# Kernel optimization log

Hardware: AMD Instinct MI355X
Metric: run time of the kernel (lower is better)

## Reference

```python
import jax, jax.numpy as jnp
import numpy as np

D = 1024
H = 16
F = 4096
EPS = 1e-6


def _layernorm(x, alpha, bias):
    # Faithful to torch: unbiased std (ddof=1), divide by (std + eps)
    mean = jnp.mean(x, axis=-1, keepdims=True)
    std = jnp.std(x, axis=-1, keepdims=True, ddof=1)
    return alpha * (x - mean) / (std + EPS) + bias


def setup_inputs() -> dict:
    key = jax.random.key(0)
    ks = jax.random.split(key, 12)
    B, S = 2, 2048
    s = 1.0 / np.sqrt(D)
    inp = {
        "x": jax.random.normal(ks[0], (B, S, D), jnp.float32),
        "mask": jnp.ones((B, 1, 1, S), jnp.int32),
        "wq": jax.random.normal(ks[1], (D, D), jnp.float32) * s,
        "bq": jnp.zeros((D,), jnp.float32),
        "wk": jax.random.normal(ks[2], (D, D), jnp.float32) * s,
        "bk": jnp.zeros((D,), jnp.float32),
        "wv": jax.random.normal(ks[3], (D, D), jnp.float32) * s,
        "bv": jnp.zeros((D,), jnp.float32),
        "wo": jax.random.normal(ks[4], (D, D), jnp.float32) * s,
        "bo": jnp.zeros((D,), jnp.float32),
        "ln1_a": jnp.ones((D,), jnp.float32),
        "ln1_b": jnp.zeros((D,), jnp.float32),
        "ln2_a": jnp.ones((D,), jnp.float32),
        "ln2_b": jnp.zeros((D,), jnp.float32),
        "w1": jax.random.normal(ks[5], (D, F), jnp.float32) * s,
        "b1": jnp.zeros((F,), jnp.float32),
        "w2": jax.random.normal(ks[6], (F, D), jnp.float32) * (1.0 / np.sqrt(F)),
        "b2": jnp.zeros((D,), jnp.float32),
    }
    return inp


def reference(x, mask, wq, bq, wk, bk, wv, bv, wo, bo,
              ln1_a, ln1_b, ln2_a, ln2_b, w1, b1, w2, b2):
    B, S, _ = x.shape
    dk = D // H
    # --- residual 1: pre-LN self-attention ---
    h = _layernorm(x, ln1_a, ln1_b)
    q = (h @ wq + bq).reshape(B, S, H, dk).transpose(0, 2, 1, 3)
    k = (h @ wk + bk).reshape(B, S, H, dk).transpose(0, 2, 1, 3)
    v = (h @ wv + bv).reshape(B, S, H, dk).transpose(0, 2, 1, 3)
    scores = jnp.einsum('bhqd,bhkd->bhqk', q, k) / jnp.sqrt(jnp.float32(dk))
    scores = jnp.where(mask == 0, jnp.float32(-1e9), scores)
    attn = jax.nn.softmax(scores, axis=-1)
    ctx = jnp.einsum('bhqk,bhkd->bhqd', attn, v)
    ctx = ctx.transpose(0, 2, 1, 3).reshape(B, S, D)
    x = x + (ctx @ wo + bo)
    # --- residual 2: pre-LN feed-forward ---
    h = _layernorm(x, ln2_a, ln2_b)
    ff = jax.nn.relu(h @ w1 + b1) @ w2 + b2
    return x + ff
```

## Files before the change

kernel.cpp:

```cpp
#include <hip/hip_runtime.h>
#include <hip/hip_bf16.h>

typedef __attribute__((ext_vector_type(8))) short bf16x8;
typedef __attribute__((ext_vector_type(4))) float f32x4;
typedef unsigned int uint32;

#define DMODEL 1024
#define SEQ    2048
#define NB     2
#define NH     16
#define HD     64
#define FDIM   4096
#define NTOK   (NB*SEQ)

__device__ __forceinline__ void async16(const void* g, void* s) {
    __builtin_amdgcn_global_load_lds((const __attribute__((address_space(1))) unsigned int*)g,
                                     (__attribute__((address_space(3))) unsigned int*)s,
                                     16, 0, 0);
}

__global__ __launch_bounds__(256) void transpose_cvt_k(const float* __restrict__ src,
                                                       __hip_bfloat16* __restrict__ dst,
                                                       int R, int C) {
    __shared__ __hip_bfloat16 tile[32][33];
    int tx = threadIdx.x, ty = threadIdx.y;
    int bx = blockIdx.x * 32, by = blockIdx.y * 32;
    for (int i = 0; i < 32; i += 8)
        tile[ty + i][tx] = __float2bfloat16(src[(size_t)(by + ty + i) * C + bx + tx]);
    __syncthreads();
    for (int i = 0; i < 32; i += 8)
        dst[(size_t)(bx + ty + i) * R + by + tx] = tile[tx][ty + i];
}

__global__ __launch_bounds__(256) void ln_kernel(const float* __restrict__ x,
                                                 const float* __restrict__ alpha,
                                                 const float* __restrict__ beta,
                                                 __hip_bfloat16* __restrict__ out) {
    const int row = blockIdx.x, tid = threadIdx.x;
    const size_t base = (size_t)row * DMODEL;
    float v[4];
    for (int e = 0; e < 4; ++e) v[e] = x[base + tid * 4 + e];
    float s1 = v[0] + v[1] + v[2] + v[3];
    float s2 = v[0]*v[0] + v[1]*v[1] + v[2]*v[2] + v[3]*v[3];
    for (int off = 32; off > 0; off >>= 1) {
        s1 += __shfl_down(s1, off);
        s2 += __shfl_down(s2, off);
    }
    __shared__ float red[8];
    int w = tid >> 6, lane = tid & 63;
    if (lane == 0) { red[w * 2] = s1; red[w * 2 + 1] = s2; }
    __syncthreads();
    if (tid == 0) {
        float a = 0.f, b = 0.f;
        for (int i = 0; i < 4; ++i) { a += red[2 * i]; b += red[2 * i + 1]; }
        red[0] = a; red[1] = b;
    }
    __syncthreads();
    s1 = red[0]; s2 = red[1];
    float mean = s1 * (1.0f / DMODEL);
    float var  = fmaxf((s2 - (float)DMODEL * mean * mean) * (1.0f / (DMODEL - 1)), 0.f);
    float inv  = 1.0f / (sqrtf(var) + 1e-6f);
    for (int e = 0; e < 4; ++e) {
        int c = tid * 4 + e;
        float y = alpha[c] * (v[e] - mean) * inv + beta[c];
        out[base + c] = __float2bfloat16(y);
    }
}

template <int EPI>
__global__ __launch_bounds__(256) void gemm_bt(const __hip_bfloat16* __restrict__ A,
                                               const __hip_bfloat16* __restrict__ Bt,
                                               const float* __restrict__ bias,
                                               const float* __restrict__ res,
                                               void* __restrict__ Cout,
                                               int M, int N, int K) {
    __shared__ alignas(16) __hip_bfloat16 As[2][128 * 32];
    __shared__ alignas(16) __hip_bfloat16 Bs[2][128 * 32];
    const int tid = threadIdx.x, l = tid & 63;
    const int w = tid >> 6;
    const int wm = w >> 1, wn = w & 1, quad = l >> 4, lc = l & 15;
    const int row0 = blockIdx.y * 128, col0 = blockIdx.x * 128;
    const int lr = l >> 2, cb = l & 3;
    const int srow = 32 * w + lr;
    const int scol = (cb ^ ((lr >> 1) & 3)) * 8;
    const int rsw  = (lc >> 1) & 3;

    f32x4 acc[4][4];
    for (int i = 0; i < 4; ++i)
        for (int j = 0; j < 4; ++j) acc[i][j] = (f32x4){0.f, 0.f, 0.f, 0.f};

    for (int c = 0; c < 2; ++c) {
        async16(A  + (size_t)(row0 + srow + 16 * c) * K + scol, (char*)&As[0][0] + w * 2048 + c * 1024);
        async16(Bt + (size_t)(col0 + srow + 16 * c) * K + scol, (char*)&Bs[0][0] + w * 2048 + c * 1024);
    }
    const int NKT = K / 32;
    for (int kt = 0; kt < NKT; ++kt) {
        const int cur = kt & 1;
        __syncthreads();
        if (kt + 1 < NKT) {
            const int k1 = (kt + 1) * 32;
            for (int c = 0; c < 2; ++c) {
                async16(A  + (size_t)(row0 + srow + 16 * c) * K + k1 + scol, (char*)&As[cur ^ 1][0] + w * 2048 + c * 1024);
                async16(Bt + (size_t)(col0 + srow + 16 * c) * K + k1 + scol, (char*)&Bs[cur ^ 1][0] + w * 2048 + c * 1024);
            }
        }
        bf16x8 af[4], bfr[4];
        for (int i = 0; i < 4; ++i) af[i]  = *(const bf16x8*)&As[cur][(64 * wm + 16 * i + lc) * 32 + (quad ^ rsw) * 8];
        for (int j = 0; j < 4; ++j) bfr[j] = *(const bf16x8*)&Bs[cur][(64 * wn + 16 * j + lc) * 32 + (quad ^ rsw) * 8];
        for (int i = 0; i < 4; ++i)
            for (int j = 0; j < 4; ++j)
                acc[i][j] = __builtin_amdgcn_mfma_f32_16x16x32_bf16(af[i], bfr[j], acc[i][j], 0, 0, 0);
    }

    __hip_bfloat16* Cb = (__hip_bfloat16*)Cout;
    float* Cf = (float*)Cout;
    for (int j = 0; j < 4; ++j) {
        int col = col0 + 64 * wn + 16 * j + lc;
        float bv = bias[col];
        for (int i = 0; i < 4; ++i) {
            int rbase = row0 + 64 * wm + 16 * i + quad * 4;
            for (int r = 0; r < 4; ++r) {
                size_t idx = (size_t)(rbase + r) * N + col;
                float vacc = acc[i][j][r] + bv;
                if (EPI == 0)      Cb[idx] = __float2bfloat16(vacc);
                else if (EPI == 1) Cb[idx] = __float2bfloat16(fmaxf(vacc, 0.f));
                else               Cf[idx] = vacc + res[idx];
            }
        }
    }
}

template <int EPI>
__global__ __launch_bounds__(512) void gemm_bt_sk(const __hip_bfloat16* __restrict__ A,
                                                  const __hip_bfloat16* __restrict__ Bt,
                                                  const float* __restrict__ bias,
                                                  const float* __restrict__ res,
                                                  void* __restrict__ Cout,
                                                  int M, int N, int K) {
    __shared__ alignas(16) char smem[65536];
    const int tid = threadIdx.x, l = tid & 63;
    const int w = tid >> 6;
    const int g = w >> 2;
    const int wl = w & 3;
    const int wm = wl >> 1, wn = wl & 1, quad = l >> 4, lc = l & 15;
    const int row0 = blockIdx.y * 128, col0 = blockIdx.x * 128;
    const int lr = l >> 2, cb = l & 3;
    const int srow = 32 * wl + lr;
    const int scol = (cb ^ ((lr >> 1) & 3)) * 8;
    const int rsw  = (lc >> 1) & 3;
    const int Kh = K >> 1;
    const int kbase = g * Kh;

    char* AsBase = smem + (size_t)g * 16384;
    char* BsBase = smem + 32768 + (size_t)g * 16384;

    f32x4 acc[4][4];
    for (int i = 0; i < 4; ++i)
        for (int j = 0; j < 4; ++j) acc[i][j] = (f32x4){0.f, 0.f, 0.f, 0.f};

    for (int c = 0; c < 2; ++c) {
        async16(A  + (size_t)(row0 + srow + 16 * c) * K + kbase + scol, AsBase + wl * 2048 + c * 1024);
        async16(Bt + (size_t)(col0 + srow + 16 * c) * K + kbase + scol, BsBase + wl * 2048 + c * 1024);
    }
    const int NKT = Kh / 32;
    for (int kt = 0; kt < NKT; ++kt) {
        const int cur = kt & 1;
        __syncthreads();
        if (kt + 1 < NKT) {
            const int k1 = kbase + (kt + 1) * 32;
            for (int c = 0; c < 2; ++c) {
                async16(A  + (size_t)(row0 + srow + 16 * c) * K + k1 + scol, AsBase + (cur ^ 1) * 8192 + wl * 2048 + c * 1024);
                async16(Bt + (size_t)(col0 + srow + 16 * c) * K + k1 + scol, BsBase + (cur ^ 1) * 8192 + wl * 2048 + c * 1024);
            }
        }
        const __hip_bfloat16* Asc = (const __hip_bfloat16*)(AsBase + cur * 8192);
        const __hip_bfloat16* Bsc = (const __hip_bfloat16*)(BsBase + cur * 8192);
        bf16x8 af[4], bfr[4];
        for (int i = 0; i < 4; ++i) af[i]  = *(const bf16x8*)&Asc[(64 * wm + 16 * i + lc) * 32 + (quad ^ rsw) * 8];
        for (int j = 0; j < 4; ++j) bfr[j] = *(const bf16x8*)&Bsc[(64 * wn + 16 * j + lc) * 32 + (quad ^ rsw) * 8];
        for (int i = 0; i < 4; ++i)
            for (int j = 0; j < 4; ++j)
                acc[i][j] = __builtin_amdgcn_mfma_f32_16x16x32_bf16(af[i], bfr[j], acc[i][j], 0, 0, 0);
    }

    __syncthreads();
    float* comb = (float*)smem;
    if (g == 1) {
        for (int j = 0; j < 4; ++j) {
            int col = 64 * wn + 16 * j + lc;
            int ccol = col ^ ((quad & 1) << 4);
            for (int i = 0; i < 4; ++i) {
                int rb = 64 * wm + 16 * i + quad * 4;
                for (int r = 0; r < 4; ++r)
                    comb[(rb + r) * 128 + ccol] = acc[i][j][r];
            }
        }
    }
    __syncthreads();
    if (g == 0) {
        __hip_bfloat16* Cb = (__hip_bfloat16*)Cout;
        float* Cf = (float*)Cout;
        for (int j = 0; j < 4; ++j) {
            int coll = 64 * wn + 16 * j + lc;
            int ccol = coll ^ ((quad & 1) << 4);
            int col  = col0 + coll;
            float bv = bias[col];
            for (int i = 0; i < 4; ++i) {
                int rbl = 64 * wm + 16 * i + quad * 4;
                for (int r = 0; r < 4; ++r) {
                    size_t idx = (size_t)(row0 + rbl + r) * N + col;
                    float vacc = acc[i][j][r] + comb[(rbl + r) * 128 + ccol] + bv;
                    if (EPI == 0)      Cb[idx] = __float2bfloat16(vacc);
                    else if (EPI == 1) Cb[idx] = __float2bfloat16(fmaxf(vacc, 0.f));
                    else               Cf[idx] = vacc + res[idx];
                }
            }
        }
    }
}

__global__ __launch_bounds__(256) void gemm_qkv(const __hip_bfloat16* __restrict__ A,
                                                const __hip_bfloat16* __restrict__ Bt,
                                                const float* __restrict__ bq,
                                                const float* __restrict__ bk,
                                                const float* __restrict__ bv,
                                                __hip_bfloat16* __restrict__ qout,
                                                __hip_bfloat16* __restrict__ kout,
                                                __hip_bfloat16* __restrict__ vTout) {
    const int K = DMODEL;
    __shared__ alignas(16) __hip_bfloat16 As[2][128 * 32];
    __shared__ alignas(16) __hip_bfloat16 Bs[2][128 * 32];
    const int tid = threadIdx.x, l = tid & 63;
    const int w = tid >> 6;
    const int wm = w >> 1, wn = w & 1, quad = l >> 4, lc = l & 15;
    const int row0 = blockIdx.y * 128, col0 = blockIdx.x * 128;
    const int lr = l >> 2, cb = l & 3;
    const int srow = 32 * w + lr;
    const int scol = (cb ^ ((lr >> 1) & 3)) * 8;
    const int rsw  = (lc >> 1) & 3;

    f32x4 acc[4][4];
    for (int i = 0; i < 4; ++i)
        for (int j = 0; j < 4; ++j) acc[i][j] = (f32x4){0.f, 0.f, 0.f, 0.f};

    for (int c = 0; c < 2; ++c) {
        async16(A  + (size_t)(row0 + srow + 16 * c) * K + scol, (char*)&As[0][0] + w * 2048 + c * 1024);
        async16(Bt + (size_t)(col0 + srow + 16 * c) * K + scol, (char*)&Bs[0][0] + w * 2048 + c * 1024);
    }
    const int NKT = K / 32;
    for (int kt = 0; kt < NKT; ++kt) {
        const int cur = kt & 1;
        __syncthreads();
        if (kt + 1 < NKT) {
            const int k1 = (kt + 1) * 32;
            for (int c = 0; c < 2; ++c) {
                async16(A  + (size_t)(row0 + srow + 16 * c) * K + k1 + scol, (char*)&As[cur ^ 1][0] + w * 2048 + c * 1024);
                async16(Bt + (size_t)(col0 + srow + 16 * c) * K + k1 + scol, (char*)&Bs[cur ^ 1][0] + w * 2048 + c * 1024);
            }
        }
        bf16x8 af[4], bfr[4];
        for (int i = 0; i < 4; ++i) af[i]  = *(const bf16x8*)&As[cur][(64 * wm + 16 * i + lc) * 32 + (quad ^ rsw) * 8];
        for (int j = 0; j < 4; ++j) bfr[j] = *(const bf16x8*)&Bs[cur][(64 * wn + 16 * j + lc) * 32 + (quad ^ rsw) * 8];
        for (int i = 0; i < 4; ++i)
            for (int j = 0; j < 4; ++j)
                acc[i][j] = __builtin_amdgcn_mfma_f32_16x16x32_bf16(af[i], bfr[j], acc[i][j], 0, 0, 0);
    }

    const int seg = col0 >> 10;
    const float* bias = (seg == 0) ? bq : (seg == 1) ? bk : bv;
    for (int j = 0; j < 4; ++j) {
        int col  = col0 + 64 * wn + 16 * j + lc;
        int colm = col & (DMODEL - 1);
        float bvx = bias[colm];
        for (int i = 0; i < 4; ++i) {
            int rbase = row0 + 64 * wm + 16 * i + quad * 4;
            for (int r = 0; r < 4; ++r) {
                int trow = rbase + r;
                float vacc = acc[i][j][r] + bvx;
                if (seg == 2) {
                    int bb = trow >> 11, s = trow & (SEQ - 1);
                    int hh = colm >> 6, d = colm & (HD - 1);
                    vTout[((size_t)(bb * NH + hh) * HD + d) * SEQ + s] = __float2bfloat16(vacc);
                } else {
                    __hip_bfloat16* dst = (seg == 0) ? qout : kout;
                    dst[(size_t)trow * DMODEL + colm] = __float2bfloat16(vacc);
                }
            }
        }
    }
}

__global__ __launch_bounds__(256) void attn_kernel(const __hip_bfloat16* __restrict__ q,
                                                   const __hip_bfloat16* __restrict__ k,
                                                   const __hip_bfloat16* __restrict__ vT,
                                                   const int* __restrict__ mask,
                                                   __hip_bfloat16* __restrict__ ctx) {
    const int qt = blockIdx.x, bh = blockIdx.y;
    const int b = bh >> 4;
    const int q0 = qt * 128;
    const int tid = threadIdx.x, w = tid >> 6, l = tid & 63, quad = l >> 4, lc = l & 15;

    __shared__ alignas(16) __hip_bfloat16 Kh[2][2][64 * 32];
    __shared__ alignas(16) __hip_bfloat16 Vh[2][2][64 * 32];

    const size_t base   = (size_t)b * SEQ * DMODEL + (size_t)(bh & 15) * HD;
    const size_t vtbase = (size_t)bh * HD * SEQ;

    bf16x8 qf[2][2];
    for (int s = 0; s < 2; ++s) {
        const __hip_bfloat16* qrow = &q[base + (size_t)(q0 + s * 64 + w * 16 + lc) * DMODEL];
        qf[s][0] = *(const bf16x8*)&qrow[quad * 8];
        qf[s][1] = *(const bf16x8*)&qrow[32 + quad * 8];
    }

    f32x4 o[2][4];
    for (int s = 0; s < 2; ++s)
        for (int dj = 0; dj < 4; ++dj) o[s][dj] = (f32x4){0.f, 0.f, 0.f, 0.f};
    float rsp2[2] = {0.f, 0.f};

    const int lr  = l >> 2, cb = l & 3;
    const int cbsw = ((cb ^ ((lr >> 1) & 3))) * 8;
    const int rsw  = (lc >> 1) & 3;
    const int b1v = (l >> 5) & 1, b0v = (l >> 4) & 1;

    for (int c = 0; c < 2; ++c) {
        const int W = w * 2 + c;
        const int rr = (W & 3) * 16 + lr, cc8 = (W >> 2) * 32 + cbsw;
        async16(&k [base   + (size_t)rr * DMODEL + cc8], (char*)&Kh[0][0][0] + W * 1024);
        async16(&vT[vtbase + (size_t)rr * SEQ + cc8],    (char*)&Vh[0][0][0] + W * 1024);
    }

    const int NT = SEQ / 64;
    for (int kt = 0; kt < NT; ++kt) {
        const int k0 = kt * 64;
        const int cur = kt & 1;

        __syncthreads();
        if (kt + 1 < NT) {
            const int k1 = k0 + 64;
            for (int c = 0; c < 2; ++c) {
                const int W = w * 2 + c;
                const int rr = (W & 3) * 16 + lr, cc8 = (W >> 2) * 32 + cbsw;
                async16(&k [base   + (size_t)(k1 + rr) * DMODEL + cc8], (char*)&Kh[cur ^ 1][0][0] + W * 1024);
                async16(&vT[vtbase + (size_t)rr * SEQ + k1 + cc8],      (char*)&Vh[cur ^ 1][0][0] + W * 1024);
            }
        }
        int4 mc[4];
        for (int jn = 0; jn < 4; ++jn)
            mc[jn] = *(const int4*)&mask[b * SEQ + k0 + jn * 16 + quad * 4];

        bf16x8 kf0[4], kf1[4];
        for (int jn = 0; jn < 4; ++jn) {
            kf0[jn] = *(const bf16x8*)&Kh[cur][0][(jn * 16 + lc) * 32 + (quad ^ rsw) * 8];
            kf1[jn] = *(const bf16x8*)&Kh[cur][1][(jn * 16 + lc) * 32 + (quad ^ rsw) * 8];
        }
        bf16x8 vf0[4], vf1[4];
        for (int dj = 0; dj < 4; ++dj) {
            vf0[dj] = *(const bf16x8*)&Vh[cur][0][(dj * 16 + lc) * 32 + (quad ^ rsw) * 8];
            vf1[dj] = *(const bf16x8*)&Vh[cur][1][(dj * 16 + lc) * 32 + (quad ^ rsw) * 8];
        }

        for (int s = 0; s < 2; ++s) {
            f32x4 sa[4];
            __builtin_amdgcn_s_setprio(1);
            for (int jn = 0; jn < 4; ++jn) {
                f32x4 z = (f32x4){0.f, 0.f, 0.f, 0.f};
                z = __builtin_amdgcn_mfma_f32_16x16x32_bf16(kf0[jn], qf[s][0], z, 0, 0, 0);
                z = __builtin_amdgcn_mfma_f32_16x16x32_bf16(kf1[jn], qf[s][1], z, 0, 0, 0);
                sa[jn] = z;
            }
            __builtin_amdgcn_s_setprio(0);

            uint32 wd[4][2];
            float accs = 0.f;
            for (int jn = 0; jn < 4; ++jn) {
                float p0 = mc[jn].x ? __expf(sa[jn][0] * 0.125f) : 0.f;
                float p1 = mc[jn].y ? __expf(sa[jn][1] * 0.125f) : 0.f;
                float p2 = mc[jn].z ? __expf(sa[jn][2] * 0.125f) : 0.f;
                float p3 = mc[jn].w ? __expf(sa[jn][3] * 0.125f) : 0.f;
                accs += (p0 + p1) + (p2 + p3);
                __hip_bfloat16 h0 = __float2bfloat16(p0), h1 = __float2bfloat16(p1);
                __hip_bfloat16 h2 = __float2bfloat16(p2), h3 = __float2bfloat16(p3);
                wd[jn][0] = (uint32)*(unsigned short*)&h0 | ((uint32)*(unsigned short*)&h1 << 16);
                wd[jn][1] = (uint32)*(unsigned short*)&h2 | ((uint32)*(unsigned short*)&h3 << 16);
            }
            rsp2[s] += accs;

            uint32 send1[4], kept[4];
            send1[0] = b1v ? wd[0][0] : wd[1][0];  kept[0] = b1v ? wd[1][0] : wd[0][0];
            send1[1] = b1v ? wd[0][1] : wd[1][1];  kept[1] = b1v ? wd[1][1] : wd[0][1];
            send1[2] = b1v ? wd[2][0] : wd[3][0];  kept[2] = b1v ? wd[3][0] : wd[2][0];
            send1[3] = b1v ? wd[2][1] : wd[3][1];  kept[3] = b1v ? wd[3][1] : wd[2][1];
            uint32 recv1[4];
            for (int t = 0; t < 4; ++t) recv1[t] = (uint32)__shfl_xor((int)send1[t], 32);
            uint32 send2[4], stay[4];
            for (int t = 0; t < 4; ++t) {
                send2[t] = (b1v == b0v) ? recv1[t] : kept[t];
                stay[t]  = (b1v == b0v) ? kept[t]  : recv1[t];
            }
            uint32 recv2[4];
            for (int t = 0; t < 4; ++t) recv2[t] = (uint32)__shfl_xor((int)send2[t], 16);
            uint32 G0[4], G1[4];
            for (int t = 0; t < 4; ++t) {
                G0[t] = b0v ? recv2[t] : stay[t];
                G1[t] = b0v ? stay[t]  : recv2[t];
            }
            union { uint32 u[4]; bf16x8 v8; } pf0, pf1;
            pf0.u[0] = G0[0]; pf0.u[1] = G0[1]; pf0.u[2] = G1[0]; pf0.u[3] = G1[1];
            pf1.u[0] = G0[2]; pf1.u[1] = G0[3]; pf1.u[2] = G1[2]; pf1.u[3] = G1[3];

            __builtin_amdgcn_s_setprio(1);
            for (int dj = 0; dj < 4; ++dj) {
                o[s][dj] = __builtin_amdgcn_mfma_f32_16x16x32_bf16(pf0.v8, vf0[dj], o[s][dj], 0, 0, 0);
                o[s][dj] = __builtin_amdgcn_mfma_f32_16x16x32_bf16(pf1.v8, vf1[dj], o[s][dj], 0, 0, 0);
            }
            __builtin_amdgcn_s_setprio(0);
        }
    }

    for (int s = 0; s < 2; ++s) {
        float rs = rsp2[s];
        rs += __shfl_xor(rs, 16);
        rs += __shfl_xor(rs, 32);
        for (int r = 0; r < 4; ++r) {
            float rq = __shfl(rs, (l & 48) | (quad * 4 + r));
            float linv = 1.0f / rq;
            int row = q0 + s * 64 + w * 16 + quad * 4 + r;
            for (int dj = 0; dj < 4; ++dj)
                ctx[base + (size_t)row * DMODEL + dj * 16 + lc] = __float2bfloat16(o[s][dj][r] * linv);
        }
    }
}

extern "C" void kernel_launch(void* const* d_in, const int* in_sizes, int n_in,
                              void* d_out, int out_size, void* d_ws, size_t ws_size,
                              hipStream_t stream) {
    const float* x    = (const float*)d_in[0];
    const int*   mask = (const int*)d_in[1];
    const float* wq = (const float*)d_in[2];
    const float* bq = (const float*)d_in[3];
    const float* wk = (const float*)d_in[4];
    const float* bk = (const float*)d_in[5];
    const float* wv = (const float*)d_in[6];
    const float* bv = (const float*)d_in[7];
    const float* wo = (const float*)d_in[8];
    const float* bo = (const float*)d_in[9];
    const float* ln1_a = (const float*)d_in[10];
    const float* ln1_b = (const float*)d_in[11];
    const float* ln2_a = (const float*)d_in[12];
    const float* ln2_b = (const float*)d_in[13];
    const float* w1 = (const float*)d_in[14];
    const float* b1 = (const float*)d_in[15];
    const float* w2 = (const float*)d_in[16];
    const float* b2 = (const float*)d_in[17];
    float* out = (float*)d_out;

    char* ws = (char*)d_ws;
    const size_t SZ_WT  = (size_t)DMODEL * DMODEL * 2;
    const size_t SZ_ACT = (size_t)NTOK * DMODEL * 2;
    const size_t SZ_WF  = (size_t)FDIM * DMODEL * 2;
    size_t off = 0;
    __hip_bfloat16* wqkvT = (__hip_bfloat16*)(ws + off); off += 3 * SZ_WT;
    __hip_bfloat16* woT   = (__hip_bfloat16*)(ws + off); off += SZ_WT;
    __hip_bfloat16* w1T   = (__hip_bfloat16*)(ws + off); off += SZ_WF;
    __hip_bfloat16* w2T   = (__hip_bfloat16*)(ws + off); off += SZ_WF;
    __hip_bfloat16* h1    = (__hip_bfloat16*)(ws + off); off += SZ_ACT;
    __hip_bfloat16* qb    = (__hip_bfloat16*)(ws + off); off += SZ_ACT;
    __hip_bfloat16* kb    = (__hip_bfloat16*)(ws + off); off += SZ_ACT;
    __hip_bfloat16* vTb   = (__hip_bfloat16*)(ws + off); off += SZ_ACT;
    __hip_bfloat16* ctx   = (__hip_bfloat16*)(ws + off); off += SZ_ACT;
    float*          x1    = (float*)(ws + off);          off += (size_t)NTOK * DMODEL * 4;
    __hip_bfloat16* h2    = (__hip_bfloat16*)(ws + off); off += SZ_ACT;
    __hip_bfloat16* ff1   = h1;

    dim3 tb(32, 8);
    transpose_cvt_k<<<dim3(32, 32), tb, 0, stream>>>(wq, wqkvT,                   DMODEL, DMODEL);
    transpose_cvt_k<<<dim3(32, 32), tb, 0, stream>>>(wk, wqkvT + 1024 * DMODEL,   DMODEL, DMODEL);
    transpose_cvt_k<<<dim3(32, 32), tb, 0, stream>>>(wv, wqkvT + 2048 * DMODEL,   DMODEL, DMODEL);
    transpose_cvt_k<<<dim3(32, 32), tb, 0, stream>>>(wo, woT, DMODEL, DMODEL);
    transpose_cvt_k<<<dim3(128, 32), tb, 0, stream>>>(w1, w1T, DMODEL, FDIM);
    transpose_cvt_k<<<dim3(32, 128), tb, 0, stream>>>(w2, w2T, FDIM, DMODEL);

    ln_kernel<<<NTOK, 256, 0, stream>>>(x, ln1_a, ln1_b, h1);

    gemm_qkv<<<dim3(3 * DMODEL / 128, NTOK / 128), 256, 0, stream>>>(h1, wqkvT, bq, bk, bv, qb, kb, vTb);

    attn_kernel<<<dim3(SEQ / 128, NB * NH), 256, 0, stream>>>(qb, kb, vTb, mask, ctx);

    gemm_bt_sk<2><<<dim3(DMODEL / 128, NTOK / 128), 512, 0, stream>>>(ctx, woT, bo, x, x1, NTOK, DMODEL, DMODEL);

    ln_kernel<<<NTOK, 256, 0, stream>>>(x1, ln2_a, ln2_b, h2);

    gemm_bt<1><<<dim3(FDIM / 128, NTOK / 128), 256, 0, stream>>>(h2, w1T, b1, nullptr, ff1, NTOK, FDIM, DMODEL);
    gemm_bt_sk<2><<<dim3(DMODEL / 128, NTOK / 128), 512, 0, stream>>>(ff1, w2T, b2, x1, out, NTOK, DMODEL, FDIM);
}
```

Baseline: 400.4 us.

## Halve attention query tile and use permlane swaps for P reshuffle

Each attention block now handles 64 query rows instead of 128, which doubles the grid so more blocks are resident across the CUs. The score-to-operand reshuffle of the probability values now uses the permlane32_swap and permlane16_swap builtins in place of __shfl_xor plus selects, cutting cross-lane instruction count. The trade-off is that each loaded K/V tile is reused for fewer query rows, so K/V global and LDS traffic per query doubles.

```diff
diff --git a/kernel.cpp b/kernel.cpp
--- a/kernel.cpp
+++ b/kernel.cpp
@@ -4,6 +4,7 @@
 typedef __attribute__((ext_vector_type(8))) short bf16x8;
 typedef __attribute__((ext_vector_type(4))) float f32x4;
 typedef unsigned int uint32;
+typedef __attribute__((ext_vector_type(2))) unsigned int uint32x2;
 
 #define DMODEL 1024
 #define SEQ    2048
@@ -297,7 +298,7 @@
                                                    __hip_bfloat16* __restrict__ ctx) {
     const int qt = blockIdx.x, bh = blockIdx.y;
     const int b = bh >> 4;
-    const int q0 = qt * 128;
+    const int q0 = qt * 64;
     const int tid = threadIdx.x, w = tid >> 6, l = tid & 63, quad = l >> 4, lc = l & 15;
 
     __shared__ alignas(16) __hip_bfloat16 Kh[2][2][64 * 32];
@@ -306,22 +307,20 @@
     const size_t base   = (size_t)b * SEQ * DMODEL + (size_t)(bh & 15) * HD;
     const size_t vtbase = (size_t)bh * HD * SEQ;
 
-    bf16x8 qf[2][2];
-    for (int s = 0; s < 2; ++s) {
-        const __hip_bfloat16* qrow = &q[base + (size_t)(q0 + s * 64 + w * 16 + lc) * DMODEL];
-        qf[s][0] = *(const bf16x8*)&qrow[quad * 8];
-        qf[s][1] = *(const bf16x8*)&qrow[32 + quad * 8];
-    }
-
-    f32x4 o[2][4];
-    for (int s = 0; s < 2; ++s)
-        for (int dj = 0; dj < 4; ++dj) o[s][dj] = (f32x4){0.f, 0.f, 0.f, 0.f};
-    float rsp2[2] = {0.f, 0.f};
+    bf16x8 qf[2];
+    {
+        const __hip_bfloat16* qrow = &q[base + (size_t)(q0 + w * 16 + lc) * DMODEL];
+        qf[0] = *(const bf16x8*)&qrow[quad * 8];
+        qf[1] = *(const bf16x8*)&qrow[32 + quad * 8];
+    }
+
+    f32x4 o[4];
+    for (int dj = 0; dj < 4; ++dj) o[dj] = (f32x4){0.f, 0.f, 0.f, 0.f};
+    float rsp = 0.f;
 
     const int lr  = l >> 2, cb = l & 3;
     const int cbsw = ((cb ^ ((lr >> 1) & 3))) * 8;
     const int rsw  = (lc >> 1) & 3;
-    const int b1v = (l >> 5) & 1, b0v = (l >> 4) & 1;
 
     for (int c = 0; c < 2; ++c) {
         const int W = w * 2 + c;
@@ -360,75 +359,58 @@
             vf1[dj] = *(const bf16x8*)&Vh[cur][1][(dj * 16 + lc) * 32 + (quad ^ rsw) * 8];
         }
 
-        for (int s = 0; s < 2; ++s) {
-            f32x4 sa[4];
-            __builtin_amdgcn_s_setprio(1);
-            for (int jn = 0; jn < 4; ++jn) {
-                f32x4 z = (f32x4){0.f, 0.f, 0.f, 0.f};
-                z = __builtin_amdgcn_mfma_f32_16x16x32_bf16(kf0[jn], qf[s][0], z, 0, 0, 0);
-                z = __builtin_amdgcn_mfma_f32_16x16x32_bf16(kf1[jn], qf[s][1], z, 0, 0, 0);
-                sa[jn] = z;
-            }
-            __builtin_amdgcn_s_setprio(0);
-
-            uint32 wd[4][2];
-            float accs = 0.f;
-            for (int jn = 0; jn < 4; ++jn) {
-                float p0 = mc[jn].x ? __expf(sa[jn][0] * 0.125f) : 0.f;
-                float p1 = mc[jn].y ? __expf(sa[jn][1] * 0.125f) : 0.f;
-                float p2 = mc[jn].z ? __expf(sa[jn][2] * 0.125f) : 0.f;
-                float p3 = mc[jn].w ? __expf(sa[jn][3] * 0.125f) : 0.f;
-                accs += (p0 + p1) + (p2 + p3);
-                __hip_bfloat16 h0 = __float2bfloat16(p0), h1 = __float2bfloat16(p1);
-                __hip_bfloat16 h2 = __float2bfloat16(p2), h3 = __float2bfloat16(p3);
-                wd[jn][0] = (uint32)*(unsigned short*)&h0 | ((uint32)*(unsigned short*)&h1 << 16);
-                wd[jn][1] = (uint32)*(unsigned short*)&h2 | ((uint32)*(unsigned short*)&h3 << 16);
-            }
-            rsp2[s] += accs;
-
-            uint32 send1[4], kept[4];
-            send1[0] = b1v ? wd[0][0] : wd[1][0];  kept[0] = b1v ? wd[1][0] : wd[0][0];
-            send1[1] = b1v ? wd[0][1] : wd[1][1];  kept[1] = b1v ? wd[1][1] : wd[0][1];
-            send1[2] = b1v ? wd[2][0] : wd[3][0];  kept[2] = b1v ? wd[3][0] : wd[2][0];
-            send1[3] = b1v ? wd[2][1] : wd[3][1];  kept[3] = b1v ? wd[3][1] : wd[2][1];
-            uint32 recv1[4];
-            for (int t = 0; t < 4; ++t) recv1[t] = (uint32)__shfl_xor((int)send1[t], 32);
-            uint32 send2[4], stay[4];
-            for (int t = 0; t < 4; ++t) {
-                send2[t] = (b1v == b0v) ? recv1[t] : kept[t];
-                stay[t]  = (b1v == b0v) ? kept[t]  : recv1[t];
-            }
-            uint32 recv2[4];
-            for (int t = 0; t < 4; ++t) recv2[t] = (uint32)__shfl_xor((int)send2[t], 16);
-            uint32 G0[4], G1[4];
-            for (int t = 0; t < 4; ++t) {
-                G0[t] = b0v ? recv2[t] : stay[t];
-                G1[t] = b0v ? stay[t]  : recv2[t];
-            }
-            union { uint32 u[4]; bf16x8 v8; } pf0, pf1;
-            pf0.u[0] = G0[0]; pf0.u[1] = G0[1]; pf0.u[2] = G1[0]; pf0.u[3] = G1[1];
-            pf1.u[0] = G0[2]; pf1.u[1] = G0[3]; pf1.u[2] = G1[2]; pf1.u[3] = G1[3];
-
-            __builtin_amdgcn_s_setprio(1);
-            for (int dj = 0; dj < 4; ++dj) {
-                o[s][dj] = __builtin_amdgcn_mfma_f32_16x16x32_bf16(pf0.v8, vf0[dj], o[s][dj], 0, 0, 0);
-                o[s][dj] = __builtin_amdgcn_mfma_f32_16x16x32_bf16(pf1.v8, vf1[dj], o[s][dj], 0, 0, 0);
-            }
-            __builtin_amdgcn_s_setprio(0);
-        }
-    }
-
-    for (int s = 0; s < 2; ++s) {
-        float rs = rsp2[s];
-        rs += __shfl_xor(rs, 16);
-        rs += __shfl_xor(rs, 32);
-        for (int r = 0; r < 4; ++r) {
-            float rq = __shfl(rs, (l & 48) | (quad * 4 + r));
-            float linv = 1.0f / rq;
-            int row = q0 + s * 64 + w * 16 + quad * 4 + r;
-            for (int dj = 0; dj < 4; ++dj)
-                ctx[base + (size_t)row * DMODEL + dj * 16 + lc] = __float2bfloat16(o[s][dj][r] * linv);
-        }
+        f32x4 sa[4];
+        __builtin_amdgcn_s_setprio(1);
+        for (int jn = 0; jn < 4; ++jn) {
+            f32x4 z = (f32x4){0.f, 0.f, 0.f, 0.f};
+            z = __builtin_amdgcn_mfma_f32_16x16x32_bf16(kf0[jn], qf[0], z, 0, 0, 0);
+            z = __builtin_amdgcn_mfma_f32_16x16x32_bf16(kf1[jn], qf[1], z, 0, 0, 0);
+            sa[jn] = z;
+        }
+        __builtin_amdgcn_s_setprio(0);
+
+        uint32 wd[4][2];
+        float accs = 0.f;
+        for (int jn = 0; jn < 4; ++jn) {
+            float p0 = mc[jn].x ? __expf(sa[jn][0] * 0.125f) : 0.f;
+            float p1 = mc[jn].y ? __expf(sa[jn][1] * 0.125f) : 0.f;
+            float p2 = mc[jn].z ? __expf(sa[jn][2] * 0.125f) : 0.f;
+            float p3 = mc[jn].w ? __expf(sa[jn][3] * 0.125f) : 0.f;
+            accs += (p0 + p1) + (p2 + p3);
+            __hip_bfloat16 h0 = __float2bfloat16(p0), h1 = __float2bfloat16(p1);
+            __hip_bfloat16 h2 = __float2bfloat16(p2), h3 = __float2bfloat16(p3);
+            wd[jn][0] = (uint32)*(unsigned short*)&h0 | ((uint32)*(unsigned short*)&h1 << 16);
+            wd[jn][1] = (uint32)*(unsigned short*)&h2 | ((uint32)*(unsigned short*)&h3 << 16);
+        }
+        rsp += accs;
+
+        union { uint32 u[4]; bf16x8 v8; } pf0, pf1;
+        for (int p = 0; p < 2; ++p) {
+            uint32x2 a = __builtin_amdgcn_permlane32_swap(wd[0][p], wd[1][p], false, false);
+            uint32x2 r = __builtin_amdgcn_permlane16_swap(a[0], a[1], false, false);
+            pf0.u[p] = r[0]; pf0.u[2 + p] = r[1];
+            uint32x2 a2 = __builtin_amdgcn_permlane32_swap(wd[2][p], wd[3][p], false, false);
+            uint32x2 r2 = __builtin_amdgcn_permlane16_swap(a2[0], a2[1], false, false);
+            pf1.u[p] = r2[0]; pf1.u[2 + p] = r2[1];
+        }
+
+        __builtin_amdgcn_s_setprio(1);
+        for (int dj = 0; dj < 4; ++dj) {
+            o[dj] = __builtin_amdgcn_mfma_f32_16x16x32_bf16(pf0.v8, vf0[dj], o[dj], 0, 0, 0);
+            o[dj] = __builtin_amdgcn_mfma_f32_16x16x32_bf16(pf1.v8, vf1[dj], o[dj], 0, 0, 0);
+        }
+        __builtin_amdgcn_s_setprio(0);
+    }
+
+    float rs = rsp;
+    rs += __shfl_xor(rs, 16);
+    rs += __shfl_xor(rs, 32);
+    for (int r = 0; r < 4; ++r) {
+        float rq = __shfl(rs, (l & 48) | (quad * 4 + r));
+        float linv = 1.0f / rq;
+        int row = q0 + w * 16 + quad * 4 + r;
+        for (int dj = 0; dj < 4; ++dj)
+            ctx[base + (size_t)row * DMODEL + dj * 16 + lc] = __float2bfloat16(o[dj][r] * linv);
     }
 }
 
@@ -485,7 +467,7 @@
 
     gemm_qkv<<<dim3(3 * DMODEL / 128, NTOK / 128), 256, 0, stream>>>(h1, wqkvT, bq, bk, bv, qb, kb, vTb);
 
-    attn_kernel<<<dim3(SEQ / 128, NB * NH), 256, 0, stream>>>(qb, kb, vTb, mask, ctx);
+    attn_kernel<<<dim3(SEQ / 64, NB * NH), 256, 0, stream>>>(qb, kb, vTb, mask, ctx);
 
     gemm_bt_sk<2><<<dim3(DMODEL / 128, NTOK / 128), 512, 0, stream>>>(ctx, woT, bo, x, x1, NTOK, DMODEL, DMODEL);
 
```

After: 412.1 us. 1.03x slower.

## Split attention key range across two wave groups and use permlane swaps

Applied to the files above, without the earlier changes.

Doubles the attention block to 512 threads; each group of four waves processes half of the key sequence with its own double-buffered K/V tiles, then partial outputs and row sums are combined through shared memory. The shuffle-based reordering of probabilities is replaced with permlane32/permlane16 swap instructions. The mask becomes an additive -inf bias folded into an fma before exp. This aims to raise per-CU wave count and latency hiding on a small grid, at the cost of a larger LDS footprint and an extra combine step.

```diff
diff --git a/kernel.cpp b/kernel.cpp
--- a/kernel.cpp
+++ b/kernel.cpp
@@ -1,9 +1,11 @@
 #include <hip/hip_runtime.h>
 #include <hip/hip_bf16.h>
+#include <math.h>
 
 typedef __attribute__((ext_vector_type(8))) short bf16x8;
 typedef __attribute__((ext_vector_type(4))) float f32x4;
 typedef unsigned int uint32;
+typedef __attribute__((ext_vector_type(2))) unsigned int uint32x2;
 
 #define DMODEL 1024
 #define SEQ    2048
@@ -290,25 +292,28 @@
     }
 }
 
-__global__ __launch_bounds__(256) void attn_kernel(const __hip_bfloat16* __restrict__ q,
-                                                   const __hip_bfloat16* __restrict__ k,
-                                                   const __hip_bfloat16* __restrict__ vT,
-                                                   const int* __restrict__ mask,
-                                                   __hip_bfloat16* __restrict__ ctx) {
+__global__ __launch_bounds__(512, 4) void attn_kernel(const __hip_bfloat16* __restrict__ q,
+                                                      const __hip_bfloat16* __restrict__ k,
+                                                      const __hip_bfloat16* __restrict__ vT,
+                                                      const int* __restrict__ mask,
+                                                      __hip_bfloat16* __restrict__ ctx) {
     const int qt = blockIdx.x, bh = blockIdx.y;
     const int b = bh >> 4;
     const int q0 = qt * 128;
     const int tid = threadIdx.x, w = tid >> 6, l = tid & 63, quad = l >> 4, lc = l & 15;
-
-    __shared__ alignas(16) __hip_bfloat16 Kh[2][2][64 * 32];
-    __shared__ alignas(16) __hip_bfloat16 Vh[2][2][64 * 32];
+    const int g = w >> 2, wl = w & 3;
+
+    __shared__ alignas(16) char smem[65536];
+    __hip_bfloat16* KhB = (__hip_bfloat16*)(smem + (size_t)g * 32768);
+    __hip_bfloat16* VhB = (__hip_bfloat16*)(smem + (size_t)g * 32768 + 16384);
 
     const size_t base   = (size_t)b * SEQ * DMODEL + (size_t)(bh & 15) * HD;
     const size_t vtbase = (size_t)bh * HD * SEQ;
+    const int gk = g * (SEQ / 2);
 
     bf16x8 qf[2][2];
     for (int s = 0; s < 2; ++s) {
-        const __hip_bfloat16* qrow = &q[base + (size_t)(q0 + s * 64 + w * 16 + lc) * DMODEL];
+        const __hip_bfloat16* qrow = &q[base + (size_t)(q0 + s * 64 + wl * 16 + lc) * DMODEL];
         qf[s][0] = *(const bf16x8*)&qrow[quad * 8];
         qf[s][1] = *(const bf16x8*)&qrow[32 + quad * 8];
     }
@@ -321,43 +326,47 @@
     const int lr  = l >> 2, cb = l & 3;
     const int cbsw = ((cb ^ ((lr >> 1) & 3))) * 8;
     const int rsw  = (lc >> 1) & 3;
-    const int b1v = (l >> 5) & 1, b0v = (l >> 4) & 1;
 
     for (int c = 0; c < 2; ++c) {
-        const int W = w * 2 + c;
+        const int W = wl * 2 + c;
         const int rr = (W & 3) * 16 + lr, cc8 = (W >> 2) * 32 + cbsw;
-        async16(&k [base   + (size_t)rr * DMODEL + cc8], (char*)&Kh[0][0][0] + W * 1024);
-        async16(&vT[vtbase + (size_t)rr * SEQ + cc8],    (char*)&Vh[0][0][0] + W * 1024);
-    }
-
-    const int NT = SEQ / 64;
+        async16(&k [base   + (size_t)(gk + rr) * DMODEL + cc8], (char*)KhB + W * 1024);
+        async16(&vT[vtbase + (size_t)rr * SEQ + gk + cc8],      (char*)VhB + W * 1024);
+    }
+
+    const int NT = SEQ / 128;
     for (int kt = 0; kt < NT; ++kt) {
-        const int k0 = kt * 64;
+        const int k0 = gk + kt * 64;
         const int cur = kt & 1;
 
         __syncthreads();
         if (kt + 1 < NT) {
             const int k1 = k0 + 64;
             for (int c = 0; c < 2; ++c) {
-                const int W = w * 2 + c;
+                const int W = wl * 2 + c;
                 const int rr = (W & 3) * 16 + lr, cc8 = (W >> 2) * 32 + cbsw;
-                async16(&k [base   + (size_t)(k1 + rr) * DMODEL + cc8], (char*)&Kh[cur ^ 1][0][0] + W * 1024);
-                async16(&vT[vtbase + (size_t)rr * SEQ + k1 + cc8],      (char*)&Vh[cur ^ 1][0][0] + W * 1024);
-            }
-        }
-        int4 mc[4];
-        for (int jn = 0; jn < 4; ++jn)
-            mc[jn] = *(const int4*)&mask[b * SEQ + k0 + jn * 16 + quad * 4];
+                async16(&k [base   + (size_t)(k1 + rr) * DMODEL + cc8], (char*)KhB + (cur ^ 1) * 8192 + W * 1024);
+                async16(&vT[vtbase + (size_t)rr * SEQ + k1 + cc8],      (char*)VhB + (cur ^ 1) * 8192 + W * 1024);
+            }
+        }
+        float mb[4][4];
+        for (int jn = 0; jn < 4; ++jn) {
+            int4 mi = *(const int4*)&mask[b * SEQ + k0 + jn * 16 + quad * 4];
+            mb[jn][0] = mi.x ? 0.f : -INFINITY;
+            mb[jn][1] = mi.y ? 0.f : -INFINITY;
+            mb[jn][2] = mi.z ? 0.f : -INFINITY;
+            mb[jn][3] = mi.w ? 0.f : -INFINITY;
+        }
 
         bf16x8 kf0[4], kf1[4];
         for (int jn = 0; jn < 4; ++jn) {
-            kf0[jn] = *(const bf16x8*)&Kh[cur][0][(jn * 16 + lc) * 32 + (quad ^ rsw) * 8];
-            kf1[jn] = *(const bf16x8*)&Kh[cur][1][(jn * 16 + lc) * 32 + (quad ^ rsw) * 8];
+            kf0[jn] = *(const bf16x8*)&KhB[(cur * 2 + 0) * 2048 + (jn * 16 + lc) * 32 + (quad ^ rsw) * 8];
+            kf1[jn] = *(const bf16x8*)&KhB[(cur * 2 + 1) * 2048 + (jn * 16 + lc) * 32 + (quad ^ rsw) * 8];
         }
         bf16x8 vf0[4], vf1[4];
         for (int dj = 0; dj < 4; ++dj) {
-            vf0[dj] = *(const bf16x8*)&Vh[cur][0][(dj * 16 + lc) * 32 + (quad ^ rsw) * 8];
-            vf1[dj] = *(const bf16x8*)&Vh[cur][1][(dj * 16 + lc) * 32 + (quad ^ rsw) * 8];
+            vf0[dj] = *(const bf16x8*)&VhB[(cur * 2 + 0) * 2048 + (dj * 16 + lc) * 32 + (quad ^ rsw) * 8];
+            vf1[dj] = *(const bf16x8*)&VhB[(cur * 2 + 1) * 2048 + (dj * 16 + lc) * 32 + (quad ^ rsw) * 8];
         }
 
         for (int s = 0; s < 2; ++s) {
@@ -374,10 +383,10 @@
             uint32 wd[4][2];
             float accs = 0.f;
             for (int jn = 0; jn < 4; ++jn) {
-                float p0 = mc[jn].x ? __expf(sa[jn][0] * 0.125f) : 0.f;
-                float p1 = mc[jn].y ? __expf(sa[jn][1] * 0.125f) : 0.f;
-                float p2 = mc[jn].z ? __expf(sa[jn][2] * 0.125f) : 0.f;
-                float p3 = mc[jn].w ? __expf(sa[jn][3] * 0.125f) : 0.f;
+                float p0 = __expf(fmaf(sa[jn][0], 0.125f, mb[jn][0]));
+                float p1 = __expf(fmaf(sa[jn][1], 0.125f, mb[jn][1]));
+                float p2 = __expf(fmaf(sa[jn][2], 0.125f, mb[jn][2]));
+                float p3 = __expf(fmaf(sa[jn][3], 0.125f, mb[jn][3]));
                 accs += (p0 + p1) + (p2 + p3);
                 __hip_bfloat16 h0 = __float2bfloat16(p0), h1 = __float2bfloat16(p1);
                 __hip_bfloat16 h2 = __float2bfloat16(p2), h3 = __float2bfloat16(p3);
@@ -386,28 +395,15 @@
             }
             rsp2[s] += accs;
 
-            uint32 send1[4], kept[4];
-            send1[0] = b1v ? wd[0][0] : wd[1][0];  kept[0] = b1v ? wd[1][0] : wd[0][0];
-            send1[1] = b1v ? wd[0][1] : wd[1][1];  kept[1] = b1v ? wd[1][1] : wd[0][1];
-            send1[2] = b1v ? wd[2][0] : wd[3][0];  kept[2] = b1v ? wd[3][0] : wd[2][0];
-            send1[3] = b1v ? wd[2][1] : wd[3][1];  kept[3] = b1v ? wd[3][1] : wd[2][1];
-            uint32 recv1[4];
-            for (int t = 0; t < 4; ++t) recv1[t] = (uint32)__shfl_xor((int)send1[t], 32);
-            uint32 send2[4], stay[4];
-            for (int t = 0; t < 4; ++t) {
-                send2[t] = (b1v == b0v) ? recv1[t] : kept[t];
-                stay[t]  = (b1v == b0v) ? kept[t]  : recv1[t];
-            }
-            uint32 recv2[4];
-            for (int t = 0; t < 4; ++t) recv2[t] = (uint32)__shfl_xor((int)send2[t], 16);
-            uint32 G0[4], G1[4];
-            for (int t = 0; t < 4; ++t) {
-                G0[t] = b0v ? recv2[t] : stay[t];
-                G1[t] = b0v ? stay[t]  : recv2[t];
-            }
             union { uint32 u[4]; bf16x8 v8; } pf0, pf1;
-            pf0.u[0] = G0[0]; pf0.u[1] = G0[1]; pf0.u[2] = G1[0]; pf0.u[3] = G1[1];
-            pf1.u[0] = G0[2]; pf1.u[1] = G0[3]; pf1.u[2] = G1[2]; pf1.u[3] = G1[3];
+            for (int p = 0; p < 2; ++p) {
+                uint32x2 a = __builtin_amdgcn_permlane32_swap(wd[0][p], wd[1][p], false, false);
+                uint32x2 r = __builtin_amdgcn_permlane16_swap(a[0], a[1], false, false);
+                pf0.u[p] = r[0]; pf0.u[2 + p] = r[1];
+                uint32x2 a2 = __builtin_amdgcn_permlane32_swap(wd[2][p], wd[3][p], false, false);
+                uint32x2 r2 = __builtin_amdgcn_permlane16_swap(a2[0], a2[1], false, false);
+                pf1.u[p] = r2[0]; pf1.u[2 + p] = r2[1];
+            }
 
             __builtin_amdgcn_s_setprio(1);
             for (int dj = 0; dj < 4; ++dj) {
@@ -418,16 +414,32 @@
         }
     }
 
-    for (int s = 0; s < 2; ++s) {
-        float rs = rsp2[s];
-        rs += __shfl_xor(rs, 16);
-        rs += __shfl_xor(rs, 32);
-        for (int r = 0; r < 4; ++r) {
-            float rq = __shfl(rs, (l & 48) | (quad * 4 + r));
-            float linv = 1.0f / rq;
-            int row = q0 + s * 64 + w * 16 + quad * 4 + r;
+    __syncthreads();
+    float* combo = (float*)smem;
+    float* crs   = (float*)(smem + 32768);
+    if (g == 1) {
+        for (int s = 0; s < 2; ++s) {
+            crs[(wl * 64 + l) * 2 + s] = rsp2[s];
             for (int dj = 0; dj < 4; ++dj)
-                ctx[base + (size_t)row * DMODEL + dj * 16 + lc] = __float2bfloat16(o[s][dj][r] * linv);
+                for (int r = 0; r < 4; ++r)
+                    combo[(s * 64 + wl * 16 + quad * 4 + r) * 64 + dj * 16 + lc] = o[s][dj][r];
+        }
+    }
+    __syncthreads();
+    if (g == 0) {
+        for (int s = 0; s < 2; ++s) {
+            float rs = rsp2[s] + crs[(wl * 64 + l) * 2 + s];
+            rs += __shfl_xor(rs, 16);
+            rs += __shfl_xor(rs, 32);
+            for (int r = 0; r < 4; ++r) {
+                float rq = __shfl(rs, (l & 48) | (quad * 4 + r));
+                float linv = 1.0f / rq;
+                int row = q0 + s * 64 + wl * 16 + quad * 4 + r;
+                for (int dj = 0; dj < 4; ++dj) {
+                    float ov = o[s][dj][r] + combo[(s * 64 + wl * 16 + quad * 4 + r) * 64 + dj * 16 + lc];
+                    ctx[base + (size_t)row * DMODEL + dj * 16 + lc] = __float2bfloat16(ov * linv);
+                }
+            }
         }
     }
 }
@@ -485,7 +497,7 @@
 
     gemm_qkv<<<dim3(3 * DMODEL / 128, NTOK / 128), 256, 0, stream>>>(h1, wqkvT, bq, bk, bv, qb, kb, vTb);
 
-    attn_kernel<<<dim3(SEQ / 128, NB * NH), 256, 0, stream>>>(qb, kb, vTb, mask, ctx);
+    attn_kernel<<<dim3(SEQ / 128, NB * NH), 512, 0, stream>>>(qb, kb, vTb, mask, ctx);
 
     gemm_bt_sk<2><<<dim3(DMODEL / 128, NTOK / 128), 512, 0, stream>>>(ctx, woT, bo, x, x1, NTOK, DMODEL, DMODEL);
 
```

New measurement: 587.3 us. 1.47x slower.
